# Performance work log

Measured on AMD Instinct MI355X. Metric: run time of the kernel, lower is better.

The kernel has to match this reference:

```python
import jax, jax.numpy as jnp
import numpy as np

EMB = 768
HEADS = 8
HEAD_DIM = EMB // HEADS  # 96


def setup_inputs() -> dict:
    key = jax.random.key(0)
    k1, k2, k3, k4, k5 = jax.random.split(key, 5)
    N, S = 2, 4096
    values = jax.random.normal(k1, (N, S, EMB), dtype=jnp.float32)
    keys = jax.random.normal(k2, (N, S, EMB), dtype=jnp.float32)
    query = jax.random.normal(k3, (N, S, EMB), dtype=jnp.float32)
    # fc_out: nn.Linear(emb_size, emb_size) -> weight [out,in], bias [out]
    bound = 1.0 / np.sqrt(EMB)
    fc_w = jax.random.uniform(k4, (EMB, EMB), dtype=jnp.float32, minval=-bound, maxval=bound)
    fc_b = jax.random.uniform(k5, (EMB,), dtype=jnp.float32, minval=-bound, maxval=bound)
    return {"values": values, "keys": keys, "query": query, "fc_w": fc_w, "fc_b": fc_b}


def reference(values, keys, query, fc_w, fc_b):
    # NOTE: original forward never uses the per-head q/k/v Linear layers;
    # it reshapes raw inputs into heads directly. We reproduce that faithfully.
    N, Sq, _ = query.shape
    # [N, S, E] -> [N, H, S, D]
    q = query.reshape(N, Sq, HEADS, HEAD_DIM).transpose(0, 2, 1, 3)
    k = keys.reshape(N, -1, HEADS, HEAD_DIM).transpose(0, 2, 1, 3)
    v = values.reshape(N, -1, HEADS, HEAD_DIM).transpose(0, 2, 1, 3)
    scale = 1.0 / np.sqrt(HEAD_DIM).astype(np.float32)
    scores = jnp.einsum('nhqd,nhkd->nhqk', q, k) * scale  # [N,H,Sq,Sk]
    p = jax.nn.softmax(scores, axis=-1)
    x = jnp.einsum('nhqk,nhkd->nhqd', p, v)  # [N,H,Sq,D]
    x = x.transpose(0, 2, 1, 3).reshape(N, Sq, EMB)
    return x @ fc_w.T + fc_b
```

## Files before the change

### kernel.cpp

```cpp
#include <hip/hip_runtime.h>
#include <hip/hip_bf16.h>

#define S_LEN 4096
#define EMB 768
#define NHEAD 8
#define HDIM 96

typedef short bf16x8 __attribute__((ext_vector_type(8)));
typedef float f32x4 __attribute__((ext_vector_type(4)));
typedef float f32x16 __attribute__((ext_vector_type(16)));

__device__ __forceinline__ short f2bf(float x) {
  union { float f; unsigned u; } v; v.f = x;
  unsigned r = v.u + 0x7fffu + ((v.u >> 16) & 1u);
  return (short)(r >> 16);
}

__device__ __forceinline__ short f2bfh(float x) {
  union { __hip_bfloat16 h; short s; } u;
  u.h = __float2bfloat16(x);
  return u.s;
}

__device__ __forceinline__ float bf2f(short s) {
  union { unsigned u; float f; } v;
  v.u = ((unsigned)(unsigned short)s) << 16;
  return v.f;
}

#define GLOAD_LDS16(gp, lp)                                              \
  __builtin_amdgcn_global_load_lds(                                      \
      (const __attribute__((address_space(1))) unsigned int*)(gp),       \
      (__attribute__((address_space(3))) unsigned int*)(lp), 16, 0, 0)

__global__ __launch_bounds__(256) void prep_kernel(const float* __restrict__ K,
                                                   const float* __restrict__ W,
                                                   const float* __restrict__ V,
                                                   short* __restrict__ KVT,
                                                   short* __restrict__ Wb) {
  __shared__ short tlbuf[6656];
  int b = blockIdx.x;
  int tid = threadIdx.x;
  if (b < 288) {
    int t = b * 256 + tid;
    size_t off = (size_t)t * 8;
    float4 a = *(const float4*)(W + off);
    float4 bq = *(const float4*)(W + off + 4);
    bf16x8 r;
    r[0]=f2bf(a.x);  r[1]=f2bf(a.y);  r[2]=f2bf(a.z);  r[3]=f2bf(a.w);
    r[4]=f2bf(bq.x); r[5]=f2bf(bq.y); r[6]=f2bf(bq.z); r[7]=f2bf(bq.w);
    *(bf16x8*)(Wb + off) = r;
    return;
  }
  if (b < 1312) {
    int bb = b - 288;
    int n = bb >> 9, h = (bb >> 6) & 7, st = bb & 63;
    int s0 = st * 64;
    const float* kp = K + ((size_t)(n * S_LEN + s0)) * EMB + h * HDIM;
    short* KVp = KVT + ((size_t)((n * NHEAD + h) * 64 + st)) * 12288;
    #pragma unroll
    for (int i = 0; i < 3; ++i) {
      int u = i * 256 + tid;
      int c = u >> 7, rem = u & 127;
      int ksub = (rem >> 6) & 1, hi2 = (rem >> 5) & 1, l31 = rem & 31;
      int key = ksub * 32 + l31;
      const float* src = kp + (size_t)key * EMB + c * 16 + hi2 * 8;
      float4 x0 = ((const float4*)src)[0];
      float4 x1 = ((const float4*)src)[1];
      bf16x8 r;
      r[0]=f2bf(x0.x); r[1]=f2bf(x0.y); r[2]=f2bf(x0.z); r[3]=f2bf(x0.w);
      r[4]=f2bf(x1.x); r[5]=f2bf(x1.y); r[6]=f2bf(x1.z); r[7]=f2bf(x1.w);
      *(bf16x8*)(KVp + (size_t)u * 8) = r;
    }
    return;
  }
  int bb = b - 1312;
  int n = bb >> 9, h = (bb >> 6) & 7, st = bb & 63;
  int s0 = st * 64;
  const float* vp = V + ((size_t)(n * S_LEN + s0)) * EMB + h * HDIM;
  #pragma unroll
  for (int k = 0; k < 6; ++k) {
    int idx = k * 256 + tid;
    int fidx = idx * 4;
    int s = fidx / 96, d = fidx % 96;
    float4 a = *(const float4*)(vp + (size_t)s * EMB + d);
    tlbuf[(d + 0) * 68 + s] = f2bf(a.x);
    tlbuf[(d + 1) * 68 + s] = f2bf(a.y);
    tlbuf[(d + 2) * 68 + s] = f2bf(a.z);
    tlbuf[(d + 3) * 68 + s] = f2bf(a.w);
  }
  __syncthreads();
  short* KVp = KVT + ((size_t)((n * NHEAD + h) * 64 + st)) * 12288 + 6144;
  #pragma unroll
  for (int i = 0; i < 3; ++i) {
    int u = i * 256 + tid;
    int slice = u / 192;
    int rem = u - slice * 192;
    int dt = rem >> 6, hi2 = (rem >> 5) & 1, d5 = rem & 31;
    int d = dt * 32 + d5;
    int kb = 16 * slice + 4 * hi2;
    short4 lo = *(const short4*)&tlbuf[d * 68 + kb];
    short4 hi4 = *(const short4*)&tlbuf[d * 68 + kb + 8];
    bf16x8 r;
    r[0]=lo.x; r[1]=lo.y; r[2]=lo.z; r[3]=lo.w;
    r[4]=hi4.x; r[5]=hi4.y; r[6]=hi4.z; r[7]=hi4.w;
    *(bf16x8*)(KVp + (size_t)u * 8) = r;
  }
}

template<int NKG>
__global__ __launch_bounds__(128, 2) void attn_kernel(const float* __restrict__ Q,
                                                      const short* __restrict__ KVT,
                                                      short* __restrict__ Xb,
                                                      short* __restrict__ Op,
                                                      float* __restrict__ lp) {
  __shared__ __align__(16) char smem[36864];
  constexpr int ITERS = S_LEN / NKG / 64;
  int L = blockIdx.x;
  int bb = L & 511;
  int kg = L >> 9;
  int h = bb & 7, j = bb >> 3;
  int n = j >> 5, qt = j & 31;
  int q0 = qt * 128;
  int tid = threadIdx.x;
  int w = tid >> 6, lane = tid & 63, l31 = lane & 31, hi = lane >> 5;

  const float kAdj = 0.14724512f;
  bf16x8 qfa[6], qfb[6];
  #pragma unroll
  for (int sub = 0; sub < 2; ++sub) {
    const float* qp = Q + ((size_t)(n * S_LEN + q0 + w * 64 + sub * 32 + l31)) * EMB
                        + h * HDIM + 8 * hi;
    #pragma unroll
    for (int c = 0; c < 6; ++c) {
      float4 a = *(const float4*)(qp + 16 * c);
      float4 bq = *(const float4*)(qp + 16 * c + 4);
      bf16x8 r;
      r[0]=f2bf(a.x*kAdj);  r[1]=f2bf(a.y*kAdj);  r[2]=f2bf(a.z*kAdj);  r[3]=f2bf(a.w*kAdj);
      r[4]=f2bf(bq.x*kAdj); r[5]=f2bf(bq.y*kAdj); r[6]=f2bf(bq.z*kAdj); r[7]=f2bf(bq.w*kAdj);
      if (sub == 0) qfa[c] = r; else qfb[c] = r;
    }
  }

  const short* gKV = KVT + ((size_t)((n * NHEAD + h) * 64 + kg * ITERS)) * 12288
                        + (size_t)(w * 6) * 512 + lane * 8;
  char* kbuf = smem;
  char* vbuf = smem + 12288;
  char* kdst = kbuf + w * 6144;
  char* vdst0 = vbuf + w * 6144;

  #pragma unroll
  for (int i = 0; i < 6; ++i) {
    GLOAD_LDS16(gKV + i * 512, kdst + i * 1024);
    GLOAD_LDS16(gKV + 6144 + i * 512, vdst0 + i * 1024);
  }
  __syncthreads();

  f32x16 oa[3], ob[3];
  #pragma unroll
  for (int dt = 0; dt < 3; ++dt) { oa[dt] = (f32x16){}; ob[dt] = (f32x16){}; }
  float tsa = 0.f, tsb = 0.f;

  int cur = 0;
  #pragma unroll 1
  for (int t = 0; t < ITERS; ++t) {
    if (t < ITERS - 1) {
      const short* src = gKV + (size_t)(t + 1) * 12288;
      char* vd = vbuf + (cur ^ 1) * 12288 + w * 6144;
      #pragma unroll
      for (int i = 0; i < 6; ++i)
        GLOAD_LDS16(src + 6144 + i * 512, vd + i * 1024);
    }

    f32x16 s0a = (f32x16){}, s1a = (f32x16){}, s0b = (f32x16){}, s1b = (f32x16){};
    __builtin_amdgcn_s_setprio(1);
    #pragma unroll
    for (int c = 0; c < 6; ++c) {
      bf16x8 kf0 = *(const bf16x8*)(kbuf + c * 2048 + lane * 16);
      bf16x8 kf1 = *(const bf16x8*)(kbuf + c * 2048 + 1024 + lane * 16);
      s0a = __builtin_amdgcn_mfma_f32_32x32x16_bf16(kf0, qfa[c], s0a, 0, 0, 0);
      s0b = __builtin_amdgcn_mfma_f32_32x32x16_bf16(kf0, qfb[c], s0b, 0, 0, 0);
      s1a = __builtin_amdgcn_mfma_f32_32x32x16_bf16(kf1, qfa[c], s1a, 0, 0, 0);
      s1b = __builtin_amdgcn_mfma_f32_32x32x16_bf16(kf1, qfb[c], s1b, 0, 0, 0);
    }
    __builtin_amdgcn_s_setprio(0);
    __syncthreads();

    if (t < ITERS - 1) {
      const short* src = gKV + (size_t)(t + 1) * 12288;
      #pragma unroll
      for (int i = 0; i < 6; ++i)
        GLOAD_LDS16(src + i * 512, kdst + i * 1024);
    }

    #pragma unroll
    for (int r = 0; r < 16; ++r) s0a[r] = __builtin_amdgcn_exp2f(s0a[r]);
    #pragma unroll
    for (int r = 0; r < 16; ++r) s1a[r] = __builtin_amdgcn_exp2f(s1a[r]);
    #pragma unroll
    for (int r = 0; r < 16; ++r) s0b[r] = __builtin_amdgcn_exp2f(s0b[r]);
    #pragma unroll
    for (int r = 0; r < 16; ++r) s1b[r] = __builtin_amdgcn_exp2f(s1b[r]);
    {
      float a0 = (s0a[0]+s0a[1])+(s0a[2]+s0a[3]), a1 = (s0a[4]+s0a[5])+(s0a[6]+s0a[7]);
      float a2 = (s0a[8]+s0a[9])+(s0a[10]+s0a[11]), a3 = (s0a[12]+s0a[13])+(s0a[14]+s0a[15]);
      float b0 = (s1a[0]+s1a[1])+(s1a[2]+s1a[3]), b1 = (s1a[4]+s1a[5])+(s1a[6]+s1a[7]);
      float b2 = (s1a[8]+s1a[9])+(s1a[10]+s1a[11]), b3 = (s1a[12]+s1a[13])+(s1a[14]+s1a[15]);
      tsa += ((a0+a1)+(a2+a3)) + ((b0+b1)+(b2+b3));
      float c0 = (s0b[0]+s0b[1])+(s0b[2]+s0b[3]), c1 = (s0b[4]+s0b[5])+(s0b[6]+s0b[7]);
      float c2 = (s0b[8]+s0b[9])+(s0b[10]+s0b[11]), c3 = (s0b[12]+s0b[13])+(s0b[14]+s0b[15]);
      float d0_ = (s1b[0]+s1b[1])+(s1b[2]+s1b[3]), d1_ = (s1b[4]+s1b[5])+(s1b[6]+s1b[7]);
      float d2_ = (s1b[8]+s1b[9])+(s1b[10]+s1b[11]), d3_ = (s1b[12]+s1b[13])+(s1b[14]+s1b[15]);
      tsb += ((c0+c1)+(c2+c3)) + ((d0_+d1_)+(d2_+d3_));
    }

    const char* vbl = vbuf + cur * 12288;
    #pragma unroll
    for (int ksub = 0; ksub < 2; ++ksub) {
      const f32x16& sa = ksub ? s1a : s0a;
      const f32x16& sb = ksub ? s1b : s0b;
      #pragma unroll
      for (int ks = 0; ks < 2; ++ks) {
        unsigned a0, a1, a2, a3, b0, b1, b2, b3;
        asm("v_cvt_pk_bf16_f32 %0, %1, %2" : "=v"(a0) : "v"(sa[8*ks+0]), "v"(sa[8*ks+1]));
        asm("v_cvt_pk_bf16_f32 %0, %1, %2" : "=v"(a1) : "v"(sa[8*ks+2]), "v"(sa[8*ks+3]));
        asm("v_cvt_pk_bf16_f32 %0, %1, %2" : "=v"(a2) : "v"(sa[8*ks+4]), "v"(sa[8*ks+5]));
        asm("v_cvt_pk_bf16_f32 %0, %1, %2" : "=v"(a3) : "v"(sa[8*ks+6]), "v"(sa[8*ks+7]));
        asm("v_cvt_pk_bf16_f32 %0, %1, %2" : "=v"(b0) : "v"(sb[8*ks+0]), "v"(sb[8*ks+1]));
        asm("v_cvt_pk_bf16_f32 %0, %1, %2" : "=v"(b1) : "v"(sb[8*ks+2]), "v"(sb[8*ks+3]));
        asm("v_cvt_pk_bf16_f32 %0, %1, %2" : "=v"(b2) : "v"(sb[8*ks+4]), "v"(sb[8*ks+5]));
        asm("v_cvt_pk_bf16_f32 %0, %1, %2" : "=v"(b3) : "v"(sb[8*ks+6]), "v"(sb[8*ks+7]));
        union { unsigned u[4]; bf16x8 v; } pa, pb;
        pa.u[0] = a0; pa.u[1] = a1; pa.u[2] = a2; pa.u[3] = a3;
        pb.u[0] = b0; pb.u[1] = b1; pb.u[2] = b2; pb.u[3] = b3;
        int slice = 2 * ksub + ks;
        __builtin_amdgcn_s_setprio(1);
        #pragma unroll
        for (int dt = 0; dt < 3; ++dt) {
          bf16x8 vf = *(const bf16x8*)(vbl + (slice * 3 + dt) * 1024 + hi * 512 + l31 * 16);
          oa[dt] = __builtin_amdgcn_mfma_f32_32x32x16_bf16(pa.v, vf, oa[dt], 0, 0, 0);
          ob[dt] = __builtin_amdgcn_mfma_f32_32x32x16_bf16(pb.v, vf, ob[dt], 0, 0, 0);
        }
        __builtin_amdgcn_s_setprio(0);
      }
    }
    __syncthreads();
    cur ^= 1;
  }

  float la = tsa + __shfl_xor(tsa, 32, 64);
  float lb = tsb + __shfl_xor(tsb, 32, 64);

  if constexpr (NKG > 1) {
    short* op = Op + (size_t)L * 12288;
    #pragma unroll
    for (int p = 0; p < 4; ++p) {
      #pragma unroll
      for (int jj = 0; jj < 4; ++jj) {
        int qra = w * 64 + 8 * p + 4 * hi + jj;
        op[(size_t)qra * 96 + l31]      = f2bfh(oa[0][4*p+jj]);
        op[(size_t)qra * 96 + 32 + l31] = f2bfh(oa[1][4*p+jj]);
        op[(size_t)qra * 96 + 64 + l31] = f2bfh(oa[2][4*p+jj]);
        int qrb = qra + 32;
        op[(size_t)qrb * 96 + l31]      = f2bfh(ob[0][4*p+jj]);
        op[(size_t)qrb * 96 + 32 + l31] = f2bfh(ob[1][4*p+jj]);
        op[(size_t)qrb * 96 + 64 + l31] = f2bfh(ob[2][4*p+jj]);
      }
    }
    if (hi == 0) {
      lp[(size_t)L * 128 + w * 64 + l31] = la;
      lp[(size_t)L * 128 + w * 64 + 32 + l31] = lb;
    }
  } else {
    __syncthreads();
    float* bcf = (float*)smem;
    if (hi == 0) {
      bcf[w * 64 + l31] = 1.0f / la;
      bcf[w * 64 + 32 + l31] = 1.0f / lb;
    }
    __syncthreads();
    #pragma unroll
    for (int p = 0; p < 4; ++p) {
      #pragma unroll
      for (int jj = 0; jj < 4; ++jj) {
        int qr = 8 * p + 4 * hi + jj;
        float iva = bcf[w * 64 + qr];
        float ivb = bcf[w * 64 + 32 + qr];
        short* xpa = Xb + ((size_t)(n * S_LEN + q0 + w * 64 + qr)) * EMB + h * HDIM + l31;
        xpa[0]  = f2bfh(oa[0][4*p+jj] * iva);
        xpa[32] = f2bfh(oa[1][4*p+jj] * iva);
        xpa[64] = f2bfh(oa[2][4*p+jj] * iva);
        short* xpb = xpa + (size_t)32 * EMB;
        xpb[0]  = f2bfh(ob[0][4*p+jj] * ivb);
        xpb[32] = f2bfh(ob[1][4*p+jj] * ivb);
        xpb[64] = f2bfh(ob[2][4*p+jj] * ivb);
      }
    }
  }
}

__global__ __launch_bounds__(256) void combine_kernel(const short* __restrict__ Op,
                                                      const float* __restrict__ lp,
                                                      short* __restrict__ Xb,
                                                      int nkg) {
  int b = blockIdx.x;
  int h = b & 7, j = b >> 3, n = j >> 5, qt = j & 31;
  int q0 = qt * 128;
  int tid = threadIdx.x;
  #pragma unroll 1
  for (int i = 0; i < 6; ++i) {
    int idx = (i * 256 + tid) * 8;
    int qr = idx / 96, d = idx - qr * 96;
    float acc[8] = {0.f, 0.f, 0.f, 0.f, 0.f, 0.f, 0.f, 0.f};
    float l = 0.f;
    for (int kg = 0; kg < nkg; ++kg) {
      size_t blk = (size_t)(kg * 512 + b);
      bf16x8 v = *(const bf16x8*)(Op + blk * 12288 + idx);
      #pragma unroll
      for (int e = 0; e < 8; ++e) acc[e] += bf2f(v[e]);
      l += lp[blk * 128 + qr];
    }
    float iv = 1.0f / l;
    bf16x8 r;
    #pragma unroll
    for (int e = 0; e < 8; ++e) r[e] = f2bfh(acc[e] * iv);
    *(bf16x8*)(Xb + ((size_t)(n * S_LEN + q0 + qr)) * EMB + h * HDIM + d) = r;
  }
}

__global__ __launch_bounds__(256) void fc_kernel(const short* __restrict__ Xb,
                                                 const short* __restrict__ Wb,
                                                 const float* __restrict__ bias,
                                                 float* __restrict__ out) {
  int m0 = blockIdx.x * 128, j0 = blockIdx.y * 64;
  int tid = threadIdx.x;
  int w = tid >> 6, lane = tid & 63, lr = lane & 15, lg = lane >> 4;
  f32x4 acc[2][4];
  #pragma unroll
  for (int sub = 0; sub < 2; ++sub)
    #pragma unroll
    for (int jt = 0; jt < 4; ++jt) acc[sub][jt] = (f32x4){0.f, 0.f, 0.f, 0.f};
  const short* xp0 = Xb + (size_t)(m0 + w * 32 + lr) * EMB + 8 * lg;
  const short* xp1 = xp0 + (size_t)16 * EMB;
  const short* wp = Wb + (size_t)(j0 + lr) * EMB + 8 * lg;
  #pragma unroll 2
  for (int kt = 0; kt < 24; ++kt) {
    bf16x8 a0 = *(const bf16x8*)(xp0 + kt * 32);
    bf16x8 a1 = *(const bf16x8*)(xp1 + kt * 32);
    #pragma unroll
    for (int jt = 0; jt < 4; ++jt) {
      bf16x8 bw = *(const bf16x8*)(wp + (size_t)(jt * 16) * EMB + kt * 32);
      acc[0][jt] = __builtin_amdgcn_mfma_f32_16x16x32_bf16(a0, bw, acc[0][jt], 0, 0, 0);
      acc[1][jt] = __builtin_amdgcn_mfma_f32_16x16x32_bf16(a1, bw, acc[1][jt], 0, 0, 0);
    }
  }
  #pragma unroll
  for (int jt = 0; jt < 4; ++jt) {
    float bb = bias[j0 + jt * 16 + lr];
    #pragma unroll
    for (int sub = 0; sub < 2; ++sub) {
      #pragma unroll
      for (int i = 0; i < 4; ++i)
        out[(size_t)(m0 + w * 32 + sub * 16 + 4 * lg + i) * EMB + j0 + jt * 16 + lr]
            = acc[sub][jt][i] + bb;
    }
  }
}

extern "C" void kernel_launch(void* const* d_in, const int* in_sizes, int n_in,
                              void* d_out, int out_size, void* d_ws, size_t ws_size,
                              hipStream_t stream) {
  (void)in_sizes; (void)n_in; (void)out_size;
  const float* V = (const float*)d_in[0];
  const float* K = (const float*)d_in[1];
  const float* Q = (const float*)d_in[2];
  const float* W = (const float*)d_in[3];
  const float* B = (const float*)d_in[4];
  float* out = (float*)d_out;
  short* KVT = (short*)d_ws;
  short* Wb  = KVT + 12582912;
  short* Xb  = Wb + 589824;
  size_t base_bytes = (size_t)(12582912 + 589824 + 6291456) * 2;
  size_t part_bytes = (size_t)2 * 512 * 12288 * 2 + (size_t)2 * 512 * 128 * 4;
  prep_kernel<<<2336, 256, 0, stream>>>(K, W, V, KVT, Wb);
  if (ws_size >= base_bytes + part_bytes) {
    short* Op = (short*)((char*)d_ws + base_bytes);
    float* lp = (float*)(Op + (size_t)2 * 512 * 12288);
    attn_kernel<2><<<1024, 128, 0, stream>>>(Q, KVT, Xb, Op, lp);
    combine_kernel<<<512, 256, 0, stream>>>(Op, lp, Xb, 2);
  } else {
    attn_kernel<1><<<512, 128, 0, stream>>>(Q, KVT, Xb, nullptr, nullptr);
  }
  fc_kernel<<<dim3(64, 12), 256, 0, stream>>>(Xb, Wb, B, out);
}
```

Baseline: 180.7 us.

## Fuse split-KV partial combine into output projection GEMM

Removes the separate combine kernel and folds its work into the fc GEMM. The GEMM loads both bf16 partial attention outputs, sums them, normalizes by the summed softmax denominators, and feeds the result straight to MFMA. This drops one launch and the write and re-read of the intermediate Xb buffer. In exchange, each of the 12 column blocks re-reads and re-combines the same partials, so partial-buffer traffic grows about twelvefold and the combine arithmetic is repeated.

```diff
diff --git a/kernel.cpp b/kernel.cpp
--- a/kernel.cpp
+++ b/kernel.cpp
@@ -299,32 +299,69 @@
   }
 }
 
-__global__ __launch_bounds__(256) void combine_kernel(const short* __restrict__ Op,
-                                                      const float* __restrict__ lp,
-                                                      short* __restrict__ Xb,
-                                                      int nkg) {
-  int b = blockIdx.x;
-  int h = b & 7, j = b >> 3, n = j >> 5, qt = j & 31;
-  int q0 = qt * 128;
+__global__ __launch_bounds__(256) void fc_fused_kernel(const short* __restrict__ Op,
+                                                       const float* __restrict__ lp,
+                                                       const short* __restrict__ Wb,
+                                                       const float* __restrict__ bias,
+                                                       float* __restrict__ out) {
+  int m0 = blockIdx.x * 128, j0 = blockIdx.y * 64;
   int tid = threadIdx.x;
-  #pragma unroll 1
-  for (int i = 0; i < 6; ++i) {
-    int idx = (i * 256 + tid) * 8;
-    int qr = idx / 96, d = idx - qr * 96;
-    float acc[8] = {0.f, 0.f, 0.f, 0.f, 0.f, 0.f, 0.f, 0.f};
-    float l = 0.f;
-    for (int kg = 0; kg < nkg; ++kg) {
-      size_t blk = (size_t)(kg * 512 + b);
-      bf16x8 v = *(const bf16x8*)(Op + blk * 12288 + idx);
-      #pragma unroll
-      for (int e = 0; e < 8; ++e) acc[e] += bf2f(v[e]);
-      l += lp[blk * 128 + qr];
-    }
-    float iv = 1.0f / l;
-    bf16x8 r;
-    #pragma unroll
-    for (int e = 0; e < 8; ++e) r[e] = f2bfh(acc[e] * iv);
-    *(bf16x8*)(Xb + ((size_t)(n * S_LEN + q0 + qr)) * EMB + h * HDIM + d) = r;
+  int w = tid >> 6, lane = tid & 63, lr = lane & 15, lg = lane >> 4;
+  int n = m0 >> 12, qt = (m0 & 4095) >> 7;
+  int bbase = (n * 32 + qt) * 8;
+  int qrow0 = w * 32 + lr, qrow1 = qrow0 + 16;
+
+  float il0[8], il1[8];
+  #pragma unroll
+  for (int h = 0; h < 8; ++h) {
+    size_t L0 = (size_t)(bbase + h), L1 = L0 + 512;
+    il0[h] = 1.0f / (lp[L0 * 128 + qrow0] + lp[L1 * 128 + qrow0]);
+    il1[h] = 1.0f / (lp[L0 * 128 + qrow1] + lp[L1 * 128 + qrow1]);
+  }
+
+  f32x4 acc[2][4];
+  #pragma unroll
+  for (int sub = 0; sub < 2; ++sub)
+    #pragma unroll
+    for (int jt = 0; jt < 4; ++jt) acc[sub][jt] = (f32x4){0.f, 0.f, 0.f, 0.f};
+
+  const short* wp = Wb + (size_t)(j0 + lr) * EMB + 8 * lg;
+  const short* opb = Op + (size_t)bbase * 12288;
+
+  #pragma unroll 2
+  for (int kt = 0; kt < 24; ++kt) {
+    int k = kt * 32 + 8 * lg;
+    int h = k / 96, d = k - h * 96;
+    const short* o0 = opb + (size_t)h * 12288;
+    const short* o1 = o0 + (size_t)512 * 12288;
+    bf16x8 pa0 = *(const bf16x8*)(o0 + qrow0 * 96 + d);
+    bf16x8 pb0 = *(const bf16x8*)(o1 + qrow0 * 96 + d);
+    bf16x8 pa1 = *(const bf16x8*)(o0 + qrow1 * 96 + d);
+    bf16x8 pb1 = *(const bf16x8*)(o1 + qrow1 * 96 + d);
+    float v0 = il0[h], v1 = il1[h];
+    bf16x8 a0, a1;
+    #pragma unroll
+    for (int e = 0; e < 8; ++e) {
+      a0[e] = f2bfh((bf2f(pa0[e]) + bf2f(pb0[e])) * v0);
+      a1[e] = f2bfh((bf2f(pa1[e]) + bf2f(pb1[e])) * v1);
+    }
+    #pragma unroll
+    for (int jt = 0; jt < 4; ++jt) {
+      bf16x8 bw = *(const bf16x8*)(wp + (size_t)(jt * 16) * EMB + kt * 32);
+      acc[0][jt] = __builtin_amdgcn_mfma_f32_16x16x32_bf16(a0, bw, acc[0][jt], 0, 0, 0);
+      acc[1][jt] = __builtin_amdgcn_mfma_f32_16x16x32_bf16(a1, bw, acc[1][jt], 0, 0, 0);
+    }
+  }
+  #pragma unroll
+  for (int jt = 0; jt < 4; ++jt) {
+    float bb = bias[j0 + jt * 16 + lr];
+    #pragma unroll
+    for (int sub = 0; sub < 2; ++sub) {
+      #pragma unroll
+      for (int i = 0; i < 4; ++i)
+        out[(size_t)(m0 + w * 32 + sub * 16 + 4 * lg + i) * EMB + j0 + jt * 16 + lr]
+            = acc[sub][jt][i] + bb;
+    }
   }
 }
 
@@ -387,9 +424,9 @@
     short* Op = (short*)((char*)d_ws + base_bytes);
     float* lp = (float*)(Op + (size_t)2 * 512 * 12288);
     attn_kernel<2><<<1024, 128, 0, stream>>>(Q, KVT, Xb, Op, lp);
-    combine_kernel<<<512, 256, 0, stream>>>(Op, lp, Xb, 2);
+    fc_fused_kernel<<<dim3(64, 12), 256, 0, stream>>>(Op, lp, Wb, B, out);
   } else {
     attn_kernel<1><<<512, 128, 0, stream>>>(Q, KVT, Xb, nullptr, nullptr);
-  }
-  fc_kernel<<<dim3(64, 12), 256, 0, stream>>>(Xb, Wb, B, out);
-}
+    fc_kernel<<<dim3(64, 12), 256, 0, stream>>>(Xb, Wb, B, out);
+  }
+}
```

Result: faster. 175.3 us (-3.0%).
